# Performance work log

Hardware: AMD Instinct MI355X
Metric: run time of the kernel (lower is better)

Reference implementation:

```python
import jax, jax.numpy as jnp
import numpy as np
from jax import lax

NUM_CHANNELS = 32
PROT_SECTION = 4
PROT_SIZE = NUM_CHANNELS * PROT_SECTION  # 128
BATCH = 128
SEQ_LEN = 8194


def setup_inputs() -> dict:
    key = jax.random.key(0)
    ks = jax.random.split(key, 6)
    input_seq = jax.random.randint(ks[0], (BATCH, SEQ_LEN), 0, 26)
    emb = jax.random.normal(ks[1], (26, 5), dtype=jnp.float32)
    conv_w = jax.random.normal(ks[2], (NUM_CHANNELS, 5, 3), dtype=jnp.float32) * 0.1
    conv_b = jnp.zeros((NUM_CHANNELS,), dtype=jnp.float32)
    W_a = jax.random.normal(ks[3], (PROT_SIZE, PROT_SIZE), dtype=jnp.float32) / np.sqrt(PROT_SIZE)
    v_a = jax.random.normal(ks[4], (PROT_SIZE,), dtype=jnp.float32)
    return {"input_seq": input_seq, "emb": emb, "conv_w": conv_w,
            "conv_b": conv_b, "W_a": W_a, "v_a": v_a}


def reference(input_seq, emb, conv_w, conv_b, W_a, v_a):
    # Embedding lookup: [B, L, 5] -> [B, 5, L]
    x = emb[input_seq].transpose(0, 2, 1)
    # Conv1d(5 -> C, k=3, valid) + bias + ReLU  (dropout is identity in eval)
    y = lax.conv_general_dilated(x, conv_w, window_strides=(1,), padding='VALID',
                                 dimension_numbers=('NCH', 'OIH', 'NCH'))
    y = jax.nn.relu(y + conv_b[None, :, None])  # [B, C, L-2]
    B, C, PL = y.shape
    S = PROT_SECTION
    new_L = PL // S
    rem = PL % S
    head = rem // 2
    tail = PL - (rem - head)
    y = y[:, :, head:tail].reshape(B, C * S, new_L)  # [B, D, N], D = C*S
    # Batched self-attention pooling (original loops over batch in Python)
    # energies[b, n] = v_a @ tanh(W_a @ H_b)
    e = jnp.einsum('d,bdn->bn', v_a, jnp.tanh(jnp.einsum('de,ben->bdn', W_a, y)))
    w = jax.nn.softmax(e, axis=-1)  # stable softmax; same math as unstable F.softmax
    ctx = jnp.einsum('bn,bdn->bd', w, y)  # [B, D]
    return ctx
```

## Files before the change

kernel.cpp:

```cpp
#include <hip/hip_runtime.h>

#define LSEQ 8194

typedef _Float16 f16x8 __attribute__((ext_vector_type(8)));
typedef _Float16 f16x2 __attribute__((ext_vector_type(2)));
typedef __attribute__((ext_vector_type(4))) float f32x4;

static __device__ __forceinline__ float tanh_fast(float x){
    float p = __expf(2.0f * x);
    float r = __builtin_amdgcn_rcpf(1.0f + p);
    return 1.0f - 2.0f * r;
}
static __device__ __forceinline__ unsigned h3relu(unsigned a, unsigned b, unsigned c){
    union { f16x2 h; unsigned u; } x, y, z, r;
    x.u = a; y.u = b; z.u = c;
    f16x2 s = x.h + y.h + z.h;
    f16x2 zero = { (_Float16)0.0f, (_Float16)0.0f };
    r.h = __builtin_elementwise_max(s, zero);
    return r.u;
}
static __device__ __forceinline__ unsigned hpack(float a, float b){
    union { f16x2 h; unsigned u; } pk;
    pk.h = (f16x2){ (_Float16)a, (_Float16)b };
    return pk.u;
}

__global__ __launch_bounds__(256, 4) void k_fused(
        const int* __restrict__ seq, const float* __restrict__ emb,
        const float* __restrict__ cw, const float* __restrict__ cb,
        const float* __restrict__ Wa, const float* __restrict__ va,
        float* __restrict__ part, float* __restrict__ stats)
{
    __shared__ __align__(16) unsigned tblH[1560];
    __shared__ unsigned short seqw16[4][260];
    __shared__ uint4 bshare[16*64];
    __shared__ float epar[4][64];
    __shared__ float red3[4][4][32];

    int tid = threadIdx.x;
    int b   = blockIdx.y;
    int x   = blockIdx.x;
    int n0  = x * 256;

    float* stage = (float*)bshare;
    if (tid < 130) stage[tid] = emb[tid];
    for (int i = tid; i < 480; i += 256) stage[130 + i] = cw[i];
    if (tid < 32)  stage[610 + tid] = cb[tid];

    const int* sb = seq + (size_t)b * LSEQ;
    for (int i = tid; i < 4*258; i += 256){
        int s = i / 258, off = i - s*258;
        seqw16[s][off] = (unsigned short)(sb[s*2048 + n0 + off] * 80);
    }

    int w = tid >> 6, lane = tid & 63;
    int m = lane & 15, q = lane >> 4;

    uint4 wfu[2][4];
    #pragma unroll
    for (int dtL = 0; dtL < 2; dtL++)
        #pragma unroll
        for (int ki = 0; ki < 4; ki++){
            const float* wrow = Wa + ((2*w + dtL)*16 + m)*128 + ki*32 + q*8;
            float4 fa = *(const float4*)wrow;
            float4 fb = *(const float4*)(wrow + 4);
            uint4 u;
            u.x = hpack(fa.x, fa.y);
            u.y = hpack(fa.z, fa.w);
            u.z = hpack(fb.x, fb.y);
            u.w = hpack(fb.z, fb.w);
            wfu[dtL][ki] = u;
        }
    float varg[2][4];
    #pragma unroll
    for (int dtL = 0; dtL < 2; dtL++)
        #pragma unroll
        for (int r = 0; r < 4; r++)
            varg[dtL][r] = va[(2*w + dtL)*16 + q*4 + r];
    __syncthreads();

    {
        const float* semb = stage;
        const float* scw  = stage + 130;
        const float* scb  = stage + 610;
        for (int gid = tid; gid < 1248; gid += 256){
            int k = gid / 416;
            int rem = gid - k*416;
            int l = rem >> 4;
            int cp = rem & 15;
            int c0 = cp*2;
            float v0 = 0.f, v1 = 0.f;
            #pragma unroll
            for (int i = 0; i < 5; i++){
                float e = semb[l*5 + i];
                v0 += scw[(c0*5 + i)*3 + k] * e;
                v1 += scw[((c0+1)*5 + i)*3 + k] * e;
            }
            if (k == 2){ v0 += scb[c0]; v1 += scb[c0+1]; }
            tblH[k*520 + l*20 + (cp & 3)*4 + (cp >> 2)] = hpack(v0, v1);
        }
    }
    __syncthreads();

    const char* tb0 = (const char*)tblH + q*16;
    const char* tb1 = tb0 + 2080;
    const char* tb2 = tb1 + 2080;

    float accp[32];
    #pragma unroll
    for (int j = 0; j < 32; j++) accp[j] = 0.f;
    float Mw = -3e38f, Sw = 0.f;

    for (int sub = 0; sub < 4; sub++){
        int row = sub*64 + w*16 + m;
        {
            unsigned o0[4], o1[4], o2[4];
            #pragma unroll
            for (int s = 0; s < 4; s++){
                o0[s] = seqw16[s][row];
                o1[s] = seqw16[s][row+1];
                o2[s] = seqw16[s][row+2];
            }
            unsigned V[4][4];
            #pragma unroll
            for (int s = 0; s < 4; s++){
                uint4 t0 = *(const uint4*)(tb0 + o0[s]);
                uint4 t1 = *(const uint4*)(tb1 + o1[s]);
                uint4 t2 = *(const uint4*)(tb2 + o2[s]);
                V[s][0] = h3relu(t0.x, t1.x, t2.x);
                V[s][1] = h3relu(t0.y, t1.y, t2.y);
                V[s][2] = h3relu(t0.z, t1.z, t2.z);
                V[s][3] = h3relu(t0.w, t1.w, t2.w);
            }
            #pragma unroll
            for (int ki = 0; ki < 4; ki++){
                uint4 o;
                o.x = __builtin_amdgcn_perm(V[1][ki], V[0][ki], 0x05040100u);
                o.y = __builtin_amdgcn_perm(V[3][ki], V[2][ki], 0x05040100u);
                o.z = __builtin_amdgcn_perm(V[1][ki], V[0][ki], 0x07060302u);
                o.w = __builtin_amdgcn_perm(V[3][ki], V[2][ki], 0x07060302u);
                bshare[(w*4 + ki)*64 + lane] = o;
            }
        }
        __syncthreads();

        f32x4 acc[2][4];
        #pragma unroll
        for (int dtL = 0; dtL < 2; dtL++)
            #pragma unroll
            for (int rg = 0; rg < 4; rg++) acc[dtL][rg] = (f32x4){0.f,0.f,0.f,0.f};
        #pragma unroll
        for (int rg = 0; rg < 4; rg++){
            #pragma unroll
            for (int ki = 0; ki < 4; ki++){
                union { uint4 u; f16x8 f; } bu, a0, a1;
                bu.u = bshare[(rg*4 + ki)*64 + lane];
                a0.u = wfu[0][ki];
                a1.u = wfu[1][ki];
                acc[0][rg] = __builtin_amdgcn_mfma_f32_16x16x32_f16(a0.f, bu.f, acc[0][rg], 0, 0, 0);
                acc[1][rg] = __builtin_amdgcn_mfma_f32_16x16x32_f16(a1.f, bu.f, acc[1][rg], 0, 0, 0);
            }
        }
        #pragma unroll
        for (int rg = 0; rg < 4; rg++){
            float ep = 0.f;
            #pragma unroll
            for (int dtL = 0; dtL < 2; dtL++){
                ep += varg[dtL][0] * tanh_fast(acc[dtL][rg][0]);
                ep += varg[dtL][1] * tanh_fast(acc[dtL][rg][1]);
                ep += varg[dtL][2] * tanh_fast(acc[dtL][rg][2]);
                ep += varg[dtL][3] * tanh_fast(acc[dtL][rg][3]);
            }
            ep += __shfl_xor(ep, 16);
            ep += __shfl_xor(ep, 32);
            if (lane < 16) epar[w][rg*16 + lane] = ep;
        }
        __syncthreads();

        float e4 = epar[0][lane] + epar[1][lane] + epar[2][lane] + epar[3][lane];
        float msub = e4;
        #pragma unroll
        for (int off = 32; off >= 1; off >>= 1)
            msub = fmaxf(msub, __shfl_xor(msub, off));
        float Mnew = fmaxf(Mw, msub);
        float alpha = __expf(Mw - Mnew);
        float wrl = __expf(e4 - Mnew);
        float ssub = wrl;
        #pragma unroll
        for (int off = 32; off >= 1; off >>= 1) ssub += __shfl_xor(ssub, off);
        Sw = alpha * Sw + ssub;
        Mw = Mnew;
        float wr = __shfl(wrl, w*16 + m);

        #pragma unroll
        for (int ki = 0; ki < 4; ki++){
            uint4 o = bshare[(w*4 + ki)*64 + lane];
            union { f16x2 h; unsigned u; } uA01, uA23, uB01, uB23;
            uA01.u = o.x; uA23.u = o.y; uB01.u = o.z; uB23.u = o.w;
            accp[ki*8 + 0] = alpha * accp[ki*8 + 0] + wr * (float)uA01.h[0];
            accp[ki*8 + 1] = alpha * accp[ki*8 + 1] + wr * (float)uA01.h[1];
            accp[ki*8 + 2] = alpha * accp[ki*8 + 2] + wr * (float)uA23.h[0];
            accp[ki*8 + 3] = alpha * accp[ki*8 + 3] + wr * (float)uA23.h[1];
            accp[ki*8 + 4] = alpha * accp[ki*8 + 4] + wr * (float)uB01.h[0];
            accp[ki*8 + 5] = alpha * accp[ki*8 + 5] + wr * (float)uB01.h[1];
            accp[ki*8 + 6] = alpha * accp[ki*8 + 6] + wr * (float)uB23.h[0];
            accp[ki*8 + 7] = alpha * accp[ki*8 + 7] + wr * (float)uB23.h[1];
        }
    }

    #pragma unroll
    for (int j = 0; j < 32; j++){
        accp[j] += __shfl_xor(accp[j], 1);
        accp[j] += __shfl_xor(accp[j], 2);
        accp[j] += __shfl_xor(accp[j], 4);
        accp[j] += __shfl_xor(accp[j], 8);
    }
    if (m == 0){
        #pragma unroll
        for (int j = 0; j < 32; j++) red3[w][q][j] = accp[j];
    }
    __syncthreads();
    if (tid < 128){
        int ki = tid >> 5, q2 = (tid >> 3) & 3, par = (tid >> 2) & 1, s = tid & 3;
        int a = ki*8 + par*4 + s;
        part[((size_t)b*8 + x)*128 + tid] =
            red3[0][q2][a] + red3[1][q2][a] + red3[2][q2][a] + red3[3][q2][a];
    }
    if (tid == 0){
        stats[((size_t)b*8 + x)*2    ] = Mw;
        stats[((size_t)b*8 + x)*2 + 1] = Sw;
    }
}

__global__ __launch_bounds__(128) void kb2_finish(const float* __restrict__ part,
        const float* __restrict__ stats, float* __restrict__ out)
{
    int b = blockIdx.x, d = threadIdx.x;
    const float* st = stats + (size_t)b*16;
    float M = -1e30f;
    #pragma unroll
    for (int x = 0; x < 8; x++) M = fmaxf(M, st[x*2]);
    float f[8], S = 0.f;
    #pragma unroll
    for (int x = 0; x < 8; x++){
        f[x] = __expf(st[x*2] - M);
        S += st[x*2+1] * f[x];
    }
    float inv = 1.0f / S;
    const float* p = part + (size_t)b*8*128 + d;
    float s = 0.f;
    #pragma unroll
    for (int x = 0; x < 8; x++) s += p[x*128] * f[x];
    out[b*128 + d] = s * inv;
}

extern "C" void kernel_launch(void* const* d_in, const int* in_sizes, int n_in,
                              void* d_out, int out_size, void* d_ws, size_t ws_size,
                              hipStream_t stream)
{
    const int*   seq = (const int*)d_in[0];
    const float* emb = (const float*)d_in[1];
    const float* cw  = (const float*)d_in[2];
    const float* cb  = (const float*)d_in[3];
    const float* Wa  = (const float*)d_in[4];
    const float* va  = (const float*)d_in[5];
    float* out = (float*)d_out;

    char* wsb = (char*)d_ws;
    float* part  = (float*)wsb;
    float* stats = (float*)(wsb + (1<<20));

    k_fused   <<<dim3(8,128), 256, 0, stream>>>(seq, emb, cw, cb, Wa, va, part, stats);
    kb2_finish<<<128,         128, 0, stream>>>(part, stats, out);
}
```

Measured before the change: 99.95 us.

## Make each wave own its positions independently, staging Wa in swizzled LDS

The block grows to 512 threads. Each of 8 waves now processes 32 sequence positions on its own, keeping the conv outputs in registers. Before, 4 waves split the projection rows and exchanged activations and energies through LDS with block-wide barriers. The full W_a is converted to fp16 into an XOR-swizzled LDS buffer and read per MFMA, and each wave keeps its own online softmax stats, emitting one partial per wave. This removes the inner-loop __syncthreads and the LDS exchanges, at the cost of 32KB of LDS per block, more LDS reads of A fragments, and a finish kernel that merges 64 partials per batch instead of 8.

```diff
diff --git a/kernel.cpp b/kernel.cpp
--- a/kernel.cpp
+++ b/kernel.cpp
@@ -25,83 +25,53 @@
     return pk.u;
 }
 
-__global__ __launch_bounds__(256, 4) void k_fused(
+__global__ __launch_bounds__(512, 6) void k_fused(
         const int* __restrict__ seq, const float* __restrict__ emb,
         const float* __restrict__ cw, const float* __restrict__ cb,
         const float* __restrict__ Wa, const float* __restrict__ va,
         float* __restrict__ part, float* __restrict__ stats)
 {
+    __shared__ __align__(16) unsigned wahL[8192];
     __shared__ __align__(16) unsigned tblH[1560];
     __shared__ unsigned short seqw16[4][260];
-    __shared__ uint4 bshare[16*64];
-    __shared__ float epar[4][64];
-    __shared__ float red3[4][4][32];
+    __shared__ __align__(16) float vaL[128];
 
     int tid = threadIdx.x;
     int b   = blockIdx.y;
     int x   = blockIdx.x;
     int n0  = x * 256;
 
-    float* stage = (float*)bshare;
-    if (tid < 130) stage[tid] = emb[tid];
-    for (int i = tid; i < 480; i += 256) stage[130 + i] = cw[i];
-    if (tid < 32)  stage[610 + tid] = cb[tid];
-
+    for (int i = tid; i < 8192; i += 512){
+        float2 t = ((const float2*)Wa)[i];
+        unsigned byteoff = ((unsigned)i << 2) ^ ((((unsigned)i >> 6) & 7u) << 4);
+        *(unsigned*)((char*)wahL + byteoff) = hpack(t.x, t.y);
+    }
+    if (tid < 128) vaL[tid] = va[tid];
     const int* sb = seq + (size_t)b * LSEQ;
-    for (int i = tid; i < 4*258; i += 256){
+    for (int i = tid; i < 4*258; i += 512){
         int s = i / 258, off = i - s*258;
         seqw16[s][off] = (unsigned short)(sb[s*2048 + n0 + off] * 80);
     }
+    for (int gid = tid; gid < 1248; gid += 512){
+        int k = gid / 416;
+        int rem = gid - k*416;
+        int l = rem >> 4;
+        int cp = rem & 15;
+        int c0 = cp*2;
+        float v0 = 0.f, v1 = 0.f;
+        #pragma unroll
+        for (int i = 0; i < 5; i++){
+            float e = emb[l*5 + i];
+            v0 += cw[(c0*5 + i)*3 + k] * e;
+            v1 += cw[((c0+1)*5 + i)*3 + k] * e;
+        }
+        if (k == 2){ v0 += cb[c0]; v1 += cb[c0+1]; }
+        tblH[k*520 + l*20 + (cp & 3)*4 + (cp >> 2)] = hpack(v0, v1);
+    }
+    __syncthreads();
 
     int w = tid >> 6, lane = tid & 63;
     int m = lane & 15, q = lane >> 4;
-
-    uint4 wfu[2][4];
-    #pragma unroll
-    for (int dtL = 0; dtL < 2; dtL++)
-        #pragma unroll
-        for (int ki = 0; ki < 4; ki++){
-            const float* wrow = Wa + ((2*w + dtL)*16 + m)*128 + ki*32 + q*8;
-            float4 fa = *(const float4*)wrow;
-            float4 fb = *(const float4*)(wrow + 4);
-            uint4 u;
-            u.x = hpack(fa.x, fa.y);
-            u.y = hpack(fa.z, fa.w);
-            u.z = hpack(fb.x, fb.y);
-            u.w = hpack(fb.z, fb.w);
-            wfu[dtL][ki] = u;
-        }
-    float varg[2][4];
-    #pragma unroll
-    for (int dtL = 0; dtL < 2; dtL++)
-        #pragma unroll
-        for (int r = 0; r < 4; r++)
-            varg[dtL][r] = va[(2*w + dtL)*16 + q*4 + r];
-    __syncthreads();
-
-    {
-        const float* semb = stage;
-        const float* scw  = stage + 130;
-        const float* scb  = stage + 610;
-        for (int gid = tid; gid < 1248; gid += 256){
-            int k = gid / 416;
-            int rem = gid - k*416;
-            int l = rem >> 4;
-            int cp = rem & 15;
-            int c0 = cp*2;
-            float v0 = 0.f, v1 = 0.f;
-            #pragma unroll
-            for (int i = 0; i < 5; i++){
-                float e = semb[l*5 + i];
-                v0 += scw[(c0*5 + i)*3 + k] * e;
-                v1 += scw[((c0+1)*5 + i)*3 + k] * e;
-            }
-            if (k == 2){ v0 += scb[c0]; v1 += scb[c0+1]; }
-            tblH[k*520 + l*20 + (cp & 3)*4 + (cp >> 2)] = hpack(v0, v1);
-        }
-    }
-    __syncthreads();
-
     const char* tb0 = (const char*)tblH + q*16;
     const char* tb1 = tb0 + 2080;
     const char* tb2 = tb1 + 2080;
@@ -111,22 +81,20 @@
     for (int j = 0; j < 32; j++) accp[j] = 0.f;
     float Mw = -3e38f, Sw = 0.f;
 
-    for (int sub = 0; sub < 4; sub++){
-        int row = sub*64 + w*16 + m;
+    #pragma unroll
+    for (int it = 0; it < 2; it++){
+        int base = w*32 + it*16 + m;
+        uint4 vfr[4];
         {
-            unsigned o0[4], o1[4], o2[4];
-            #pragma unroll
-            for (int s = 0; s < 4; s++){
-                o0[s] = seqw16[s][row];
-                o1[s] = seqw16[s][row+1];
-                o2[s] = seqw16[s][row+2];
-            }
             unsigned V[4][4];
             #pragma unroll
             for (int s = 0; s < 4; s++){
-                uint4 t0 = *(const uint4*)(tb0 + o0[s]);
-                uint4 t1 = *(const uint4*)(tb1 + o1[s]);
-                uint4 t2 = *(const uint4*)(tb2 + o2[s]);
+                unsigned oa = seqw16[s][base];
+                unsigned ob = seqw16[s][base+1];
+                unsigned oc = seqw16[s][base+2];
+                uint4 t0 = *(const uint4*)(tb0 + oa);
+                uint4 t1 = *(const uint4*)(tb1 + ob);
+                uint4 t2 = *(const uint4*)(tb2 + oc);
                 V[s][0] = h3relu(t0.x, t1.x, t2.x);
                 V[s][1] = h3relu(t0.y, t1.y, t2.y);
                 V[s][2] = h3relu(t0.z, t1.z, t2.z);
@@ -139,72 +107,56 @@
                 o.y = __builtin_amdgcn_perm(V[3][ki], V[2][ki], 0x05040100u);
                 o.z = __builtin_amdgcn_perm(V[1][ki], V[0][ki], 0x07060302u);
                 o.w = __builtin_amdgcn_perm(V[3][ki], V[2][ki], 0x07060302u);
-                bshare[(w*4 + ki)*64 + lane] = o;
+                vfr[ki] = o;
             }
         }
-        __syncthreads();
-
-        f32x4 acc[2][4];
-        #pragma unroll
-        for (int dtL = 0; dtL < 2; dtL++)
-            #pragma unroll
-            for (int rg = 0; rg < 4; rg++) acc[dtL][rg] = (f32x4){0.f,0.f,0.f,0.f};
-        #pragma unroll
-        for (int rg = 0; rg < 4; rg++){
+
+        float ep = 0.f;
+        #pragma unroll
+        for (int dt = 0; dt < 8; dt++){
+            f32x4 acc = (f32x4){0.f, 0.f, 0.f, 0.f};
             #pragma unroll
             for (int ki = 0; ki < 4; ki++){
-                union { uint4 u; f16x8 f; } bu, a0, a1;
-                bu.u = bshare[(rg*4 + ki)*64 + lane];
-                a0.u = wfu[0][ki];
-                a1.u = wfu[1][ki];
-                acc[0][rg] = __builtin_amdgcn_mfma_f32_16x16x32_f16(a0.f, bu.f, acc[0][rg], 0, 0, 0);
-                acc[1][rg] = __builtin_amdgcn_mfma_f32_16x16x32_f16(a1.f, bu.f, acc[1][rg], 0, 0, 0);
+                unsigned abyte = (unsigned)((dt*16 + m)*256 + ki*64 + q*16)
+                               ^ (((unsigned)(m & 7)) << 4);
+                union { uint4 u; f16x8 f; } af, bf;
+                af.u = *(const uint4*)((const char*)wahL + abyte);
+                bf.u = vfr[ki];
+                acc = __builtin_amdgcn_mfma_f32_16x16x32_f16(af.f, bf.f, acc, 0, 0, 0);
             }
-        }
-        #pragma unroll
-        for (int rg = 0; rg < 4; rg++){
-            float ep = 0.f;
-            #pragma unroll
-            for (int dtL = 0; dtL < 2; dtL++){
-                ep += varg[dtL][0] * tanh_fast(acc[dtL][rg][0]);
-                ep += varg[dtL][1] * tanh_fast(acc[dtL][rg][1]);
-                ep += varg[dtL][2] * tanh_fast(acc[dtL][rg][2]);
-                ep += varg[dtL][3] * tanh_fast(acc[dtL][rg][3]);
-            }
-            ep += __shfl_xor(ep, 16);
-            ep += __shfl_xor(ep, 32);
-            if (lane < 16) epar[w][rg*16 + lane] = ep;
-        }
-        __syncthreads();
-
-        float e4 = epar[0][lane] + epar[1][lane] + epar[2][lane] + epar[3][lane];
-        float msub = e4;
-        #pragma unroll
-        for (int off = 32; off >= 1; off >>= 1)
+            const f32x4 vg = *(const f32x4*)&vaL[dt*16 + q*4];
+            ep += vg[0] * tanh_fast(acc[0]);
+            ep += vg[1] * tanh_fast(acc[1]);
+            ep += vg[2] * tanh_fast(acc[2]);
+            ep += vg[3] * tanh_fast(acc[3]);
+        }
+        ep += __shfl_xor(ep, 16);
+        ep += __shfl_xor(ep, 32);
+
+        float msub = ep;
+        #pragma unroll
+        for (int off = 8; off >= 1; off >>= 1)
             msub = fmaxf(msub, __shfl_xor(msub, off));
         float Mnew = fmaxf(Mw, msub);
         float alpha = __expf(Mw - Mnew);
-        float wrl = __expf(e4 - Mnew);
+        float wrl = __expf(ep - Mnew);
         float ssub = wrl;
         #pragma unroll
-        for (int off = 32; off >= 1; off >>= 1) ssub += __shfl_xor(ssub, off);
+        for (int off = 8; off >= 1; off >>= 1) ssub += __shfl_xor(ssub, off);
         Sw = alpha * Sw + ssub;
         Mw = Mnew;
-        float wr = __shfl(wrl, w*16 + m);
 
         #pragma unroll
         for (int ki = 0; ki < 4; ki++){
-            uint4 o = bshare[(w*4 + ki)*64 + lane];
-            union { f16x2 h; unsigned u; } uA01, uA23, uB01, uB23;
-            uA01.u = o.x; uA23.u = o.y; uB01.u = o.z; uB23.u = o.w;
-            accp[ki*8 + 0] = alpha * accp[ki*8 + 0] + wr * (float)uA01.h[0];
-            accp[ki*8 + 1] = alpha * accp[ki*8 + 1] + wr * (float)uA01.h[1];
-            accp[ki*8 + 2] = alpha * accp[ki*8 + 2] + wr * (float)uA23.h[0];
-            accp[ki*8 + 3] = alpha * accp[ki*8 + 3] + wr * (float)uA23.h[1];
-            accp[ki*8 + 4] = alpha * accp[ki*8 + 4] + wr * (float)uB01.h[0];
-            accp[ki*8 + 5] = alpha * accp[ki*8 + 5] + wr * (float)uB01.h[1];
-            accp[ki*8 + 6] = alpha * accp[ki*8 + 6] + wr * (float)uB23.h[0];
-            accp[ki*8 + 7] = alpha * accp[ki*8 + 7] + wr * (float)uB23.h[1];
+            union { uint4 u; f16x2 h[4]; } vv; vv.u = vfr[ki];
+            accp[ki*8 + 0] = alpha * accp[ki*8 + 0] + wrl * (float)vv.h[0][0];
+            accp[ki*8 + 1] = alpha * accp[ki*8 + 1] + wrl * (float)vv.h[0][1];
+            accp[ki*8 + 2] = alpha * accp[ki*8 + 2] + wrl * (float)vv.h[1][0];
+            accp[ki*8 + 3] = alpha * accp[ki*8 + 3] + wrl * (float)vv.h[1][1];
+            accp[ki*8 + 4] = alpha * accp[ki*8 + 4] + wrl * (float)vv.h[2][0];
+            accp[ki*8 + 5] = alpha * accp[ki*8 + 5] + wrl * (float)vv.h[2][1];
+            accp[ki*8 + 6] = alpha * accp[ki*8 + 6] + wrl * (float)vv.h[3][0];
+            accp[ki*8 + 7] = alpha * accp[ki*8 + 7] + wrl * (float)vv.h[3][1];
         }
     }
 
@@ -215,20 +167,20 @@
         accp[j] += __shfl_xor(accp[j], 4);
         accp[j] += __shfl_xor(accp[j], 8);
     }
+    size_t chunk = ((size_t)b*8 + x)*8 + w;
     if (m == 0){
-        #pragma unroll
-        for (int j = 0; j < 32; j++) red3[w][q][j] = accp[j];
-    }
-    __syncthreads();
-    if (tid < 128){
-        int ki = tid >> 5, q2 = (tid >> 3) & 3, par = (tid >> 2) & 1, s = tid & 3;
-        int a = ki*8 + par*4 + s;
-        part[((size_t)b*8 + x)*128 + tid] =
-            red3[0][q2][a] + red3[1][q2][a] + red3[2][q2][a] + red3[3][q2][a];
-    }
-    if (tid == 0){
-        stats[((size_t)b*8 + x)*2    ] = Mw;
-        stats[((size_t)b*8 + x)*2 + 1] = Sw;
+        float* pd = part + chunk*128;
+        #pragma unroll
+        for (int ki = 0; ki < 4; ki++){
+            float4 lo = { accp[ki*8+0], accp[ki*8+1], accp[ki*8+2], accp[ki*8+3] };
+            float4 hi = { accp[ki*8+4], accp[ki*8+5], accp[ki*8+6], accp[ki*8+7] };
+            *(float4*)(pd + ki*32 + q*8)     = lo;
+            *(float4*)(pd + ki*32 + q*8 + 4) = hi;
+        }
+    }
+    if (lane == 0){
+        stats[chunk*2    ] = Mw;
+        stats[chunk*2 + 1] = Sw;
     }
 }
 
@@ -236,21 +188,19 @@
         const float* __restrict__ stats, float* __restrict__ out)
 {
     int b = blockIdx.x, d = threadIdx.x;
-    const float* st = stats + (size_t)b*16;
-    float M = -1e30f;
-    #pragma unroll
-    for (int x = 0; x < 8; x++) M = fmaxf(M, st[x*2]);
-    float f[8], S = 0.f;
-    #pragma unroll
-    for (int x = 0; x < 8; x++){
-        f[x] = __expf(st[x*2] - M);
-        S += st[x*2+1] * f[x];
+    const float* st = stats + (size_t)b*128;
+    float M = -3e38f;
+    #pragma unroll 8
+    for (int c = 0; c < 64; c++) M = fmaxf(M, st[c*2]);
+    const float* p = part + (size_t)b*64*128 + d;
+    float S = 0.f, s = 0.f;
+    #pragma unroll 4
+    for (int c = 0; c < 64; c++){
+        float f = __expf(st[c*2] - M);
+        S += st[c*2+1] * f;
+        s += p[c*128] * f;
     }
     float inv = 1.0f / S;
-    const float* p = part + (size_t)b*8*128 + d;
-    float s = 0.f;
-    #pragma unroll
-    for (int x = 0; x < 8; x++) s += p[x*128] * f[x];
     out[b*128 + d] = s * inv;
 }
 
@@ -268,8 +218,8 @@
 
     char* wsb = (char*)d_ws;
     float* part  = (float*)wsb;
-    float* stats = (float*)(wsb + (1<<20));
-
-    k_fused   <<<dim3(8,128), 256, 0, stream>>>(seq, emb, cw, cb, Wa, va, part, stats);
+    float* stats = (float*)(wsb + (8<<20));
+
+    k_fused   <<<dim3(8,128), 512, 0, stream>>>(seq, emb, cw, cb, Wa, va, part, stats);
     kb2_finish<<<128,         128, 0, stream>>>(part, stats, out);
 }
```

Result: slower. 108.8 us (+8.9%).
